# Kernel tuning notes

Measured on AMD Instinct MI355X. Metric: run time of the kernel, lower is better.

The kernel has to match this reference:

```python
import jax, jax.numpy as jnp
import numpy as np

B, T = 64, 512
IN, OUT, H = 256, 256, 1024


def _lstm_cell(x, h, c, Wih, Whh, bih, bhh):
    # PyTorch LSTMCell: gates = x@Wih^T + bih + h@Whh^T + bhh, order i,f,g,o
    gates = x @ Wih.T + bih + h @ Whh.T + bhh
    i, f, g, o = jnp.split(gates, 4, axis=-1)
    c_new = jax.nn.sigmoid(f) * c + jax.nn.sigmoid(i) * jnp.tanh(g)
    h_new = jax.nn.sigmoid(o) * jnp.tanh(c_new)
    return h_new, c_new


def setup_inputs() -> dict:
    key = jax.random.key(0)
    ks = jax.random.split(key, 12)
    s = 1.0 / np.sqrt(H)  # torch default uniform(-1/sqrt(H), 1/sqrt(H))
    u = lambda k, shp: jax.random.uniform(k, shp, jnp.float32, -s, s)
    return {
        "z": jax.random.normal(ks[0], (B, H), jnp.float32),
        "x": jax.random.normal(ks[1], (B, T, IN), jnp.float32),
        "Wih0": u(ks[2], (4 * H, IN)),
        "Whh0": u(ks[3], (4 * H, H)),
        "bih0": u(ks[4], (4 * H,)),
        "bhh0": u(ks[5], (4 * H,)),
        "Wih1": u(ks[6], (4 * H, H)),
        "Whh1": u(ks[7], (4 * H, H)),
        "bih1": u(ks[8], (4 * H,)),
        "bhh1": u(ks[9], (4 * H,)),
        "Wlin": u(ks[10], (OUT, H)),
        "blin": u(ks[11], (OUT,)),
    }


def reference(z, x, Wih0, Whh0, bih0, bhh0, Wih1, Whh1, bih1, bhh1, Wlin, blin):
    # Teacher-forcing unroll: h_t[l] init to z, c_t[l] init to 0, first input is zeros,
    # then input at step t+1 is x[:, t].
    x_tb = jnp.swapaxes(x, 0, 1)  # [T, B, IN]
    c0_init = jnp.zeros_like(z)

    def step(carry, x_t):
        cur_in, h0, c0, h1, c1 = carry
        h0, c0 = _lstm_cell(cur_in, h0, c0, Wih0, Whh0, bih0, bhh0)
        h1, c1 = _lstm_cell(h0, h1, c1, Wih1, Whh1, bih1, bhh1)
        out_t = h1 @ Wlin.T + blin  # [B, OUT]
        return (x_t, h0, c0, h1, c1), out_t

    init = (jnp.zeros((z.shape[0], Wih0.shape[1]), z.dtype), z, c0_init, z, c0_init)
    _, outs = jax.lax.scan(step, init, x_tb)  # outs: [T, B, OUT]
    return jnp.swapaxes(outs, 0, 1)  # [B, T, OUT]
```

## Files before the change

### kernel.cpp

```cpp
#include <hip/hip_runtime.h>
#include <hip/hip_bf16.h>
#include <math.h>


typedef __attribute__((ext_vector_type(8))) short bf16x8;
typedef __attribute__((ext_vector_type(4))) float f32x4;
typedef unsigned long long u64;

__device__ __forceinline__ float sigm(float v) {
  return 1.f / (1.f + __expf(-v));
}
__device__ __forceinline__ float ftanh(float v) {
  return 2.f / (1.f + __expf(-2.f * v)) - 1.f;
}

__device__ __forceinline__ unsigned short bf16_bits(float v) {
  __hip_bfloat16 hb = __float2bfloat16(v);
  unsigned short us;
  __builtin_memcpy(&us, &hb, 2);
  return us;
}

__device__ __forceinline__ void vstore_bf16(__hip_bfloat16* p, float v) {
  *(volatile unsigned short*)p = bf16_bits(v);
}


__global__ __launch_bounds__(256) void prep_w0(const float* __restrict__ Wih0,
                                               const float* __restrict__ Whh0,
                                               __hip_bfloat16* __restrict__ W0) {
  const unsigned n = 4096u * 1280u;
  for (unsigned d = blockIdx.x * blockDim.x + threadIdx.x; d < n;
       d += blockDim.x * gridDim.x) {
    unsigned r = d / 1280u;
    unsigned k = d - r * 1280u;
    unsigned u = r >> 2, g = r & 3u;
    unsigned srow = g * 1024u + u;
    float v = (k < 256u) ? Wih0[(size_t)srow * 256u + k]
                         : Whh0[(size_t)srow * 1024u + (k - 256u)];
    W0[d] = __float2bfloat16(v);
  }
}

__global__ __launch_bounds__(256) void prep_w1(const float* __restrict__ Wih1,
                                               const float* __restrict__ Whh1,
                                               const float* __restrict__ Wlin,
                                               __hip_bfloat16* __restrict__ W1) {
  const unsigned n = 4352u * 2048u;
  for (unsigned d = blockIdx.x * blockDim.x + threadIdx.x; d < n;
       d += blockDim.x * gridDim.x) {
    unsigned r = d >> 11;
    unsigned k = d & 2047u;
    float v;
    if (r < 4096u) {
      unsigned u = r >> 2, g = r & 3u;
      unsigned srow = g * 1024u + u;
      v = (k < 1024u) ? Wih1[(size_t)srow * 1024u + k]
                      : Whh1[(size_t)srow * 1024u + (k - 1024u)];
    } else {
      unsigned o = r - 4096u;
      v = (k < 1024u) ? 0.f : Wlin[(size_t)o * 1024u + (k - 1024u)];
    }
    W1[d] = __float2bfloat16(v);
  }
}

__global__ __launch_bounds__(256) void prep_x(const float* __restrict__ x,
                                              __hip_bfloat16* __restrict__ xbf) {
  const unsigned n = 512u * 64u * 256u;
  for (unsigned d = blockIdx.x * blockDim.x + threadIdx.x; d < n;
       d += blockDim.x * gridDim.x) {
    unsigned t = d >> 14;
    unsigned b = (d >> 8) & 63u;
    unsigned k = d & 255u;
    float v = (t == 0u) ? 0.f : x[((size_t)b * 512u + (t - 1u)) * 256u + k];
    xbf[d] = __float2bfloat16(v);
  }
}

__global__ __launch_bounds__(256) void prep_misc(
    const float* __restrict__ bih0, const float* __restrict__ bhh0,
    const float* __restrict__ bih1, const float* __restrict__ bhh1,
    const float* __restrict__ z, float* __restrict__ b0, float* __restrict__ b1,
    __hip_bfloat16* __restrict__ h0buf, __hip_bfloat16* __restrict__ h1buf) {
  for (int i = blockIdx.x * blockDim.x + threadIdx.x; i < 73728;
       i += blockDim.x * gridDim.x) {
    if (i < 4096) {
      int u = i >> 2, g = i & 3;
      b0[i] = bih0[g * 1024 + u] + bhh0[g * 1024 + u];
    } else if (i < 8192) {
      int r = i - 4096;
      int u = r >> 2, g = r & 3;
      b1[r] = bih1[g * 1024 + u] + bhh1[g * 1024 + u];
    } else {
      int j = i - 8192;
      float zv = z[j];
      vstore_bf16(h0buf + j, zv);
      vstore_bf16(h1buf + 2 * 65536 + j, zv);
    }
  }
}


__device__ __forceinline__ void do_proj(const __hip_bfloat16* __restrict__ h1p,
                                        const bf16x8* wp, float (*red)[16][68],
                                        const float* __restrict__ blin,
                                        float* __restrict__ out, int pcol,
                                        int pbat, int t_out, int tid, int w,
                                        int col, int kq) {
  f32x4 a0 = {0.f, 0.f, 0.f, 0.f};
  const __hip_bfloat16* ab =
      h1p + ((size_t)((pbat << 4) + col) << 10) + (w << 7) + (kq << 3);
#pragma unroll
  for (int c = 0; c < 4; ++c) {
    bf16x8 f = *(const bf16x8*)(ab + (c << 5));
    a0 = __builtin_amdgcn_mfma_f32_16x16x32_bf16(f, wp[c], a0, 0, 0, 0);
  }
  *(f32x4*)&red[w][col][(kq << 2)] = a0;
  __syncthreads();
  if (tid < 256) {
    int o_l = tid & 15, b = tid >> 4;
    float v = blin[(pcol << 4) + o_l];
#pragma unroll
    for (int ww = 0; ww < 8; ++ww) v += red[ww][o_l][b];
    out[(((size_t)((pbat << 4) + b) << 9) + (size_t)t_out) * 256 + (pcol << 4) +
        o_l] = v;
  }
}


__global__ __launch_bounds__(512) void k_persist(
    const __hip_bfloat16* __restrict__ xbf, const __hip_bfloat16* __restrict__ W0,
    const __hip_bfloat16* __restrict__ W1, const float* __restrict__ b0,
    const float* __restrict__ b1, const float* __restrict__ blin,
    __hip_bfloat16* __restrict__ h0buf, __hip_bfloat16* __restrict__ h1buf,
    float* __restrict__ out, unsigned* __restrict__ flags) {
  const int tid = threadIdx.x;
  const int lane = tid & 63;
  const int w = tid >> 6;
  const int bid = blockIdx.x;
  const int cb = bid << 4;
  const int col = lane & 15;
  const int kq = lane >> 4;
  const int n = cb + col;
  const bool isproj = (bid >= 64 && bid < 128);
  const int pcol = bid & 15;
  const int pbat = (bid >> 4) & 3;

  __shared__ int s_lead;
  {
    unsigned* lead = flags + 256;
    if (tid == 0) {
      unsigned xcc = 0;
      asm volatile("s_getreg_b32 %0, hwreg(HW_REG_XCC_ID)" : "=s"(xcc));
      unsigned old = __hip_atomic_fetch_add(&lead[xcc & 7u], 1u,
                                            __ATOMIC_RELAXED,
                                            __HIP_MEMORY_SCOPE_AGENT);
      s_lead = (old == 0u || bid >= 248) ? 1 : 0;
    }
  }

  bf16x8 wa[5], wb[8], wp[4];
  {
    const __hip_bfloat16* p = W0 + (size_t)n * 1280 + w * 160 + (kq << 3);
#pragma unroll
    for (int c = 0; c < 5; ++c) wa[c] = *(const bf16x8*)(p + (c << 5));
  }
  {
    const __hip_bfloat16* p = W1 + ((size_t)n << 11) + (w << 8) + (kq << 3);
#pragma unroll
    for (int c = 0; c < 8; ++c) wb[c] = *(const bf16x8*)(p + (c << 5));
  }
  if (isproj) {
    const __hip_bfloat16* p = W1 +
        ((size_t)(4096 + (pcol << 4) + col) << 11) + 1024 + (w << 7) + (kq << 3);
#pragma unroll
    for (int c = 0; c < 4; ++c) wp[c] = *(const bf16x8*)(p + (c << 5));
  }

  const int u_l = tid & 3, bq = tid >> 2;
  float bias0[4], bias1[4];
  if (tid < 256) {
#pragma unroll
    for (int g = 0; g < 4; ++g) {
      bias0[g] = b0[cb + (u_l << 2) + g];
      bias1[g] = b1[cb + (u_l << 2) + g];
    }
  }
  float c0v = 0.f, c1v = 0.f;

  __shared__ float red[8][16][68];

  __syncthreads();

  for (int t = 0; t < 512; ++t) {
    const __hip_bfloat16* h0prev = h0buf + ((size_t)(t & 1) << 16);
    const __hip_bfloat16* h0cur = h0buf + ((size_t)((t + 1) & 1) << 16);
    const __hip_bfloat16* h1prev = h1buf + ((size_t)((t + 2) % 3) << 16);

    {
      f32x4 a0 = {0.f, 0.f, 0.f, 0.f}, a1 = a0, a2 = a0, a3 = a0;
#pragma unroll
      for (int c = 0; c < 5; ++c) {
        const int k0 = w * 160 + (c << 5);
        const __hip_bfloat16* ab;
        size_t rs;
        if (k0 < 256) {
          ab = xbf + ((size_t)t << 14) + k0 + (kq << 3);
          rs = 256;
        } else {
          ab = h0prev + (k0 - 256) + (kq << 3);
          rs = 1024;
        }
        bf16x8 f0 = *(const bf16x8*)(ab + (size_t)col * rs);
        bf16x8 f1 = *(const bf16x8*)(ab + (size_t)(16 + col) * rs);
        bf16x8 f2 = *(const bf16x8*)(ab + (size_t)(32 + col) * rs);
        bf16x8 f3 = *(const bf16x8*)(ab + (size_t)(48 + col) * rs);
        a0 = __builtin_amdgcn_mfma_f32_16x16x32_bf16(f0, wa[c], a0, 0, 0, 0);
        a1 = __builtin_amdgcn_mfma_f32_16x16x32_bf16(f1, wa[c], a1, 0, 0, 0);
        a2 = __builtin_amdgcn_mfma_f32_16x16x32_bf16(f2, wa[c], a2, 0, 0, 0);
        a3 = __builtin_amdgcn_mfma_f32_16x16x32_bf16(f3, wa[c], a3, 0, 0, 0);
      }
      *(f32x4*)&red[w][col][(kq << 2)] = a0;
      *(f32x4*)&red[w][col][16 + (kq << 2)] = a1;
      *(f32x4*)&red[w][col][32 + (kq << 2)] = a2;
      *(f32x4*)&red[w][col][48 + (kq << 2)] = a3;
    }
    __syncthreads();
    if (tid < 256) {
      float gg[4];
#pragma unroll
      for (int g = 0; g < 4; ++g) {
        float v = bias0[g];
#pragma unroll
        for (int ww = 0; ww < 8; ++ww) v += red[ww][(u_l << 2) + g][bq];
        gg[g] = v;
      }
      float cn = sigm(gg[1]) * c0v + sigm(gg[0]) * ftanh(gg[2]);
      c0v = cn;
      vstore_bf16((__hip_bfloat16*)h0cur + ((size_t)bq << 10) + (cb >> 2) + u_l,
                  sigm(gg[3]) * ftanh(cn));
    }
    __syncthreads();

    if (w == 0) {
      __builtin_amdgcn_sched_barrier(0);
      if (s_lead) {
        __builtin_amdgcn_fence(__ATOMIC_ACQUIRE, "agent");
      } else {
        asm volatile("buffer_inv" ::: "memory");
      }
      __builtin_amdgcn_sched_barrier(0);
    }
    __syncthreads();

    if (isproj && t >= 2) {
      do_proj(h1buf + (((size_t)((t + 1) % 3)) << 16), wp, red, blin, out,
              pcol, pbat, t - 2, tid, w, col, kq);
    } else if (w < 2 && t < 511) {
      const char* px = (const char*)(xbf + ((size_t)(t + 1) << 14));
      const int idx = (w << 6) | lane;
#pragma unroll
      for (int i = 0; i < 4; ++i) {
        unsigned v = *(const unsigned*)(px + ((idx + (i << 7)) << 6));
        asm volatile("" ::"v"(v));
      }
    }

    __builtin_amdgcn_s_waitcnt(0);
    __syncthreads();
    if (tid == 0)
      __hip_atomic_store(&flags[bid], (unsigned)(t + 1), __ATOMIC_RELAXED,
                         __HIP_MEMORY_SCOPE_AGENT);
    if (w == 0) {
      const unsigned tgt = (unsigned)(t + 1);
      const u64* fq = (const u64*)flags;
      for (;;) {
        u64 q0 = __hip_atomic_load(&fq[2 * lane], __ATOMIC_RELAXED,
                                   __HIP_MEMORY_SCOPE_AGENT);
        u64 q1 = __hip_atomic_load(&fq[2 * lane + 1], __ATOMIC_RELAXED,
                                   __HIP_MEMORY_SCOPE_AGENT);
        int ok = ((unsigned)q0 >= tgt) & ((unsigned)(q0 >> 32) >= tgt) &
                 ((unsigned)q1 >= tgt) & ((unsigned)(q1 >> 32) >= tgt);
        if (__all(ok)) break;
        __builtin_amdgcn_s_sleep(1);
      }
    }
    __syncthreads();

    {
      const __hip_bfloat16* ab =
          ((w < 4) ? h0cur : h1prev) + ((w & 3) << 8) + (kq << 3);
      f32x4 a0 = {0.f, 0.f, 0.f, 0.f}, a1 = a0, a2 = a0, a3 = a0;
#pragma unroll
      for (int c = 0; c < 8; ++c) {
        const __hip_bfloat16* p = ab + (c << 5);
        bf16x8 f0 = *(const bf16x8*)(p + ((size_t)col << 10));
        bf16x8 f1 = *(const bf16x8*)(p + ((size_t)(16 + col) << 10));
        bf16x8 f2 = *(const bf16x8*)(p + ((size_t)(32 + col) << 10));
        bf16x8 f3 = *(const bf16x8*)(p + ((size_t)(48 + col) << 10));
        a0 = __builtin_amdgcn_mfma_f32_16x16x32_bf16(f0, wb[c], a0, 0, 0, 0);
        a1 = __builtin_amdgcn_mfma_f32_16x16x32_bf16(f1, wb[c], a1, 0, 0, 0);
        a2 = __builtin_amdgcn_mfma_f32_16x16x32_bf16(f2, wb[c], a2, 0, 0, 0);
        a3 = __builtin_amdgcn_mfma_f32_16x16x32_bf16(f3, wb[c], a3, 0, 0, 0);
      }
      *(f32x4*)&red[w][col][(kq << 2)] = a0;
      *(f32x4*)&red[w][col][16 + (kq << 2)] = a1;
      *(f32x4*)&red[w][col][32 + (kq << 2)] = a2;
      *(f32x4*)&red[w][col][48 + (kq << 2)] = a3;
    }
    __syncthreads();
    if (tid < 256) {
      float gg[4];
#pragma unroll
      for (int g = 0; g < 4; ++g) {
        float v = bias1[g];
#pragma unroll
        for (int ww = 0; ww < 8; ++ww) v += red[ww][(u_l << 2) + g][bq];
        gg[g] = v;
      }
      float cn = sigm(gg[1]) * c1v + sigm(gg[0]) * ftanh(gg[2]);
      c1v = cn;
      vstore_bf16(h1buf + ((size_t)(t % 3) << 16) + ((size_t)bq << 10) +
                      (cb >> 2) + u_l,
                  sigm(gg[3]) * ftanh(cn));
    }
    __syncthreads();
  }

  __builtin_amdgcn_s_waitcnt(0);
  __syncthreads();
  if (tid == 0)
    __hip_atomic_store(&flags[bid], 513u, __ATOMIC_RELAXED,
                       __HIP_MEMORY_SCOPE_AGENT);
  if (!isproj) return;
  if (w == 0) {
    const u64* fq = (const u64*)flags;
    for (;;) {
      u64 q0 = __hip_atomic_load(&fq[2 * lane], __ATOMIC_RELAXED,
                                 __HIP_MEMORY_SCOPE_AGENT);
      u64 q1 = __hip_atomic_load(&fq[2 * lane + 1], __ATOMIC_RELAXED,
                                 __HIP_MEMORY_SCOPE_AGENT);
      int ok = ((unsigned)q0 >= 513u) & ((unsigned)(q0 >> 32) >= 513u) &
               ((unsigned)q1 >= 513u) & ((unsigned)(q1 >> 32) >= 513u);
      if (__all(ok)) break;
      __builtin_amdgcn_s_sleep(1);
    }
    __builtin_amdgcn_fence(__ATOMIC_ACQUIRE, "agent");
  }
  __syncthreads();
  do_proj(h1buf, wp, red, blin, out, pcol, pbat, 510, tid, w, col, kq);
  __syncthreads();
  do_proj(h1buf + ((size_t)1 << 16), wp, red, blin, out, pcol, pbat, 511, tid,
          w, col, kq);
}


extern "C" void kernel_launch(void* const* d_in, const int* in_sizes, int n_in,
                              void* d_out, int out_size, void* d_ws, size_t ws_size,
                              hipStream_t stream) {
  const float* z = (const float*)d_in[0];
  const float* x = (const float*)d_in[1];
  const float* Wih0 = (const float*)d_in[2];
  const float* Whh0 = (const float*)d_in[3];
  const float* bih0 = (const float*)d_in[4];
  const float* bhh0 = (const float*)d_in[5];
  const float* Wih1 = (const float*)d_in[6];
  const float* Whh1 = (const float*)d_in[7];
  const float* bih1 = (const float*)d_in[8];
  const float* bhh1 = (const float*)d_in[9];
  const float* Wlin = (const float*)d_in[10];
  const float* blin = (const float*)d_in[11];
  float* out = (float*)d_out;

  char* ws = (char*)d_ws;
  __hip_bfloat16* W0 = (__hip_bfloat16*)(ws);
  __hip_bfloat16* W1 = (__hip_bfloat16*)(ws + 10485760);
  __hip_bfloat16* xbf = (__hip_bfloat16*)(ws + 28311552);
  float* b0 = (float*)(ws + 45088768);
  float* b1 = (float*)(ws + 45105152);
  __hip_bfloat16* h0buf = (__hip_bfloat16*)(ws + 45121536);
  __hip_bfloat16* h1buf = (__hip_bfloat16*)(ws + 45383680);
  unsigned* flags = (unsigned*)(ws + 45776896);

  hipMemsetAsync(flags, 0, 4096, stream);
  prep_w0<<<4096, 256, 0, stream>>>(Wih0, Whh0, W0);
  prep_w1<<<4096, 256, 0, stream>>>(Wih1, Whh1, Wlin, W1);
  prep_x<<<4096, 256, 0, stream>>>(x, xbf);
  prep_misc<<<288, 256, 0, stream>>>(bih0, bhh0, bih1, bhh1, z, b0, b1, h0buf,
                                     h1buf);

  k_persist<<<256, 512, 0, stream>>>(xbf, W0, W1, b0, b1, blin, h0buf, h1buf,
                                     out, flags);
}
```

Before: 9.436 ms.

## Use per-XCD aggregator blocks for the grid barrier instead of all-block polling

Replaces the all-blocks-poll-all-flags grid barrier with a two-level scheme. One leader block per XCD polls the 256 per-block flags, issues an agent-scope acquire fence and then writes a per-XCD release word. The other blocks spin only on that single word and invalidate their local cache (or fence, for bid<8). The goal is less polling traffic on the flags and cheaper cache invalidation per step. The cost is an extra hop of latency through the leader on every one of the 512 steps, and correctness now depends on the XCC-ID grouping and on the flags+272 region being zeroed.

```diff
diff --git a/kernel.cpp b/kernel.cpp
--- a/kernel.cpp
+++ b/kernel.cpp
@@ -147,16 +147,17 @@
   const int pcol = bid & 15;
   const int pbat = (bid >> 4) & 3;
 
-  __shared__ int s_lead;
+  __shared__ int s_agg, s_xcd;
   {
     unsigned* lead = flags + 256;
     if (tid == 0) {
       unsigned xcc = 0;
       asm volatile("s_getreg_b32 %0, hwreg(HW_REG_XCC_ID)" : "=s"(xcc));
-      unsigned old = __hip_atomic_fetch_add(&lead[xcc & 7u], 1u,
-                                            __ATOMIC_RELAXED,
+      xcc &= 7u;
+      unsigned old = __hip_atomic_fetch_add(&lead[xcc], 1u, __ATOMIC_RELAXED,
                                             __HIP_MEMORY_SCOPE_AGENT);
-      s_lead = (old == 0u || bid >= 248) ? 1 : 0;
+      s_agg = (old == 0u) ? 1 : 0;
+      s_xcd = (int)xcc;
     }
   }
 
@@ -192,6 +193,8 @@
   __shared__ float red[8][16][68];
 
   __syncthreads();
+
+  unsigned* rel = flags + 272 + (s_xcd << 4);
 
   for (int t = 0; t < 512; ++t) {
     const __hip_bfloat16* h0prev = h0buf + ((size_t)(t & 1) << 16);
@@ -243,17 +246,6 @@
     }
     __syncthreads();
 
-    if (w == 0) {
-      __builtin_amdgcn_sched_barrier(0);
-      if (s_lead) {
-        __builtin_amdgcn_fence(__ATOMIC_ACQUIRE, "agent");
-      } else {
-        asm volatile("buffer_inv" ::: "memory");
-      }
-      __builtin_amdgcn_sched_barrier(0);
-    }
-    __syncthreads();
-
     if (isproj && t >= 2) {
       do_proj(h1buf + (((size_t)((t + 1) % 3)) << 16), wp, red, blin, out,
               pcol, pbat, t - 2, tid, w, col, kq);
@@ -274,16 +266,33 @@
                          __HIP_MEMORY_SCOPE_AGENT);
     if (w == 0) {
       const unsigned tgt = (unsigned)(t + 1);
-      const u64* fq = (const u64*)flags;
-      for (;;) {
-        u64 q0 = __hip_atomic_load(&fq[2 * lane], __ATOMIC_RELAXED,
-                                   __HIP_MEMORY_SCOPE_AGENT);
-        u64 q1 = __hip_atomic_load(&fq[2 * lane + 1], __ATOMIC_RELAXED,
-                                   __HIP_MEMORY_SCOPE_AGENT);
-        int ok = ((unsigned)q0 >= tgt) & ((unsigned)(q0 >> 32) >= tgt) &
-                 ((unsigned)q1 >= tgt) & ((unsigned)(q1 >> 32) >= tgt);
-        if (__all(ok)) break;
-        __builtin_amdgcn_s_sleep(1);
+      if (s_agg) {
+        const u64* fq = (const u64*)flags;
+        for (;;) {
+          u64 q0 = __hip_atomic_load(&fq[2 * lane], __ATOMIC_RELAXED,
+                                     __HIP_MEMORY_SCOPE_AGENT);
+          u64 q1 = __hip_atomic_load(&fq[2 * lane + 1], __ATOMIC_RELAXED,
+                                     __HIP_MEMORY_SCOPE_AGENT);
+          int ok = ((unsigned)q0 >= tgt) & ((unsigned)(q0 >> 32) >= tgt) &
+                   ((unsigned)q1 >= tgt) & ((unsigned)(q1 >> 32) >= tgt);
+          if (__all(ok)) break;
+          __builtin_amdgcn_s_sleep(1);
+        }
+        __builtin_amdgcn_fence(__ATOMIC_ACQUIRE, "agent");
+        if (lane == 0)
+          __hip_atomic_store(rel, tgt, __ATOMIC_RELAXED,
+                             __HIP_MEMORY_SCOPE_AGENT);
+      } else {
+        while (__hip_atomic_load(rel, __ATOMIC_RELAXED,
+                                 __HIP_MEMORY_SCOPE_AGENT) < tgt)
+          __builtin_amdgcn_s_sleep(1);
+        if (bid < 8) {
+          __builtin_amdgcn_fence(__ATOMIC_ACQUIRE, "agent");
+        } else {
+          __builtin_amdgcn_sched_barrier(0);
+          asm volatile("buffer_inv" ::: "memory");
+          __builtin_amdgcn_sched_barrier(0);
+        }
       }
     }
     __syncthreads();
@@ -333,8 +342,7 @@
   if (tid == 0)
     __hip_atomic_store(&flags[bid], 513u, __ATOMIC_RELAXED,
                        __HIP_MEMORY_SCOPE_AGENT);
-  if (!isproj) return;
-  if (w == 0) {
+  if (w == 0 && s_agg) {
     const u64* fq = (const u64*)flags;
     for (;;) {
       u64 q0 = __hip_atomic_load(&fq[2 * lane], __ATOMIC_RELAXED,
@@ -346,6 +354,16 @@
       if (__all(ok)) break;
       __builtin_amdgcn_s_sleep(1);
     }
+    __builtin_amdgcn_fence(__ATOMIC_ACQUIRE, "agent");
+    if (lane == 0)
+      __hip_atomic_store(rel, 513u, __ATOMIC_RELAXED,
+                         __HIP_MEMORY_SCOPE_AGENT);
+  }
+  if (!isproj) return;
+  if (w == 0 && !s_agg) {
+    while (__hip_atomic_load(rel, __ATOMIC_RELAXED,
+                             __HIP_MEMORY_SCOPE_AGENT) < 513u)
+      __builtin_amdgcn_s_sleep(1);
     __builtin_amdgcn_fence(__ATOMIC_ACQUIRE, "agent");
   }
   __syncthreads();
```

Result: faster. 8.848 ms (-6.2%).
